# Kernel tuning notes

Measured on AMD Instinct MI355X. Metric: run time of the kernel, lower is better.

## Reference

```python
import jax, jax.numpy as jnp
import numpy as np

EMBED_DIM = 64
CODEBOOK_SIZE = 2048
COMMITMENT_COST = 1.0


def setup_inputs() -> dict:
    key = jax.random.key(0)
    k1, k2 = jax.random.split(key)
    inputs = jax.random.normal(k1, (32, 2048, EMBED_DIM), dtype=jnp.float32)
    embeddings = jax.random.normal(k2, (EMBED_DIM, CODEBOOK_SIZE), dtype=jnp.float32)
    return {"inputs": inputs, "embeddings": embeddings}


def reference(inputs, embeddings):
    # inference path (training=False): deterministic argmin quantization.
    D = embeddings.shape[0]
    K = embeddings.shape[1]
    flat = inputs.reshape(-1, D)                       # [N, D]
    similarity = flat @ embeddings                     # [N, K]
    distances = (jnp.sum(flat * flat, axis=1, keepdims=True)
                 - 2.0 * similarity
                 + jnp.sum(embeddings * embeddings, axis=0, keepdims=True))
    # gumbel layer with temperature 0 / eval mode -> argmax(-dist) == argmin(dist)
    flat_indices = jnp.argmax(-distances, axis=1)      # [N]
    encodings = jax.nn.one_hot(flat_indices, K, dtype=jnp.float32)  # [N, K]
    encoding_indices = flat_indices.reshape(inputs.shape[:-1])      # [B, T]
    quantized = jnp.take(embeddings.T, encoding_indices, axis=0)    # [B, T, D]
    e_latent_loss = jnp.mean(jnp.square(jax.lax.stop_gradient(quantized) - inputs))
    loss = e_latent_loss * COMMITMENT_COST
    return quantized, encodings, encoding_indices, loss
```

## Files before the change

kernel.cpp:

```cpp
#include <hip/hip_runtime.h>

#define N_ROWS 65536
#define DDIM   64
#define KCODES 2048
#define NB     128
#define CHUNK  256
#define NCHUNK (KCODES / CHUNK)
#define TAU    0.05f

#define Q_OFF    ((size_t)0)
#define ENC_OFF  ((size_t)N_ROWS * DDIM)
#define IDX_OFF  (ENC_OFF + (size_t)N_ROWS * KCODES)
#define LOSS_OFF (IDX_OFF + (size_t)N_ROWS)
#define INV_ND (1.0f / ((float)N_ROWS * (float)DDIM))

#define WS_ESQ_OFF   (524288)
#define WS_FLAGS_OFF (532480)

typedef __attribute__((ext_vector_type(8))) short short8;
typedef __attribute__((ext_vector_type(4))) float f32x4;

__device__ __forceinline__ unsigned short f2bf(float f) {
    unsigned u = __float_as_uint(f);
    u += 0x7FFFu + ((u >> 16) & 1u);
    return (unsigned short)(u >> 16);
}
__device__ __forceinline__ float bf2f(unsigned short h) {
    return __uint_as_float(((unsigned)h) << 16);
}

__global__ void vq_prep(const float* __restrict__ emb, char* __restrict__ ws,
                        float* __restrict__ out) {
    int t = blockIdx.x * 256 + threadIdx.x;
    int code = t & (KCODES - 1);
    int d    = t >> 11;
    float v = emb[(size_t)d * KCODES + code];
    unsigned short hi = f2bf(v);
    unsigned short lo = f2bf(v - bf2f(hi));
    int ch = code >> 8;
    int lc = code & 255;
    int kk = d ^ ((code & 7) << 3);
    short* base = (short*)ws + (size_t)ch * 32768 + lc * 64 + kk;
    base[0]     = (short)hi;
    base[16384] = (short)lo;
    if (t < KCODES) {
        float s = 0.f;
        for (int dd = 0; dd < DDIM; ++dd) {
            float e = emb[(size_t)dd * KCODES + t];
            s += e * e;
        }
        ((float*)(ws + WS_ESQ_OFF))[t] = s;
    }
    if (t == 0) out[LOSS_OFF] = 0.f;
}

__launch_bounds__(256, 2)
__global__ void vq_main(const float* __restrict__ x, const float* __restrict__ emb,
                        const char* __restrict__ ws, int* __restrict__ flags,
                        float* __restrict__ out) {
    __shared__ __align__(16) short Bs[32768];
    const int tid = threadIdx.x;
    const int l = tid & 63, w = tid >> 6;
    const int q = l >> 4, c = l & 15;
    const int r0 = blockIdx.x * NB;
    const float* esq = (const float*)(ws + WS_ESQ_OFF);

    short8 ah0[2], ah1[2], al0[2], al1[2];
    #pragma unroll
    for (int rt = 0; rt < 2; ++rt) {
        int row = r0 + w * 32 + rt * 16 + c;
        const float4* xr = (const float4*)(x + (size_t)row * DDIM);
        float4 f0 = xr[q * 2],     f1 = xr[q * 2 + 1];
        float4 f2 = xr[8 + q * 2], f3 = xr[8 + q * 2 + 1];
        float a0[8] = {f0.x,f0.y,f0.z,f0.w,f1.x,f1.y,f1.z,f1.w};
        float a1[8] = {f2.x,f2.y,f2.z,f2.w,f3.x,f3.y,f3.z,f3.w};
        #pragma unroll
        for (int j = 0; j < 8; ++j) {
            unsigned short h0 = f2bf(a0[j]);
            ah0[rt][j] = (short)h0;
            al0[rt][j] = (short)f2bf(a0[j] - bf2f(h0));
            unsigned short h1 = f2bf(a1[j]);
            ah1[rt][j] = (short)h1;
            al1[rt][j] = (short)f2bf(a1[j] - bf2f(h1));
        }
    }

    float m1[8], m2[8], m3[8]; int i1[8], i2[8];
    #pragma unroll
    for (int s = 0; s < 8; ++s) {
        m1[s] = 3.4e38f; m2[s] = 3.4e38f; m3[s] = 3.4e38f; i1[s] = 0; i2[s] = 0;
    }

    for (int ch = 0; ch < NCHUNK; ++ch) {
        const int kc = ch * CHUNK;
        __builtin_amdgcn_sched_barrier(0);
        asm volatile("s_waitcnt lgkmcnt(0)" ::: "memory");
        __builtin_amdgcn_s_barrier();
        __builtin_amdgcn_sched_barrier(0);
        {
            const int4* g4 = (const int4*)(ws + (size_t)ch * 65536);
            int4* s4 = (int4*)Bs;
            #pragma unroll
            for (int i = 0; i < 16; ++i) s4[i * 256 + tid] = g4[i * 256 + tid];
        }
        __builtin_amdgcn_sched_barrier(0);
        asm volatile("s_waitcnt lgkmcnt(0)" ::: "memory");
        __builtin_amdgcn_s_barrier();
        __builtin_amdgcn_sched_barrier(0);

        const int swz = (c & 7) << 3;
        float* ebase = out + ENC_OFF + (size_t)r0 * KCODES + kc;
        const f32x4 z = {0.f, 0.f, 0.f, 0.f};
        for (int t = 0; t < 16; ++t) {
            #pragma unroll
            for (int jj = 0; jj < 2; ++jj) {
                int s   = (t * 2 + jj) * 256 + tid;
                int row = s >> 6;
                int c4  = s & 63;
                __builtin_nontemporal_store(
                    z, (f32x4*)(ebase + (size_t)row * KCODES + (c4 << 2)));
            }
            int codeL = t * 16 + c;
            const short* ph = Bs + codeL * 64;
            const short* pl = ph + 16384;
            int k0 = (q * 8) ^ swz;
            int k1 = (32 + q * 8) ^ swz;
            short8 bh0 = *(const short8*)(ph + k0);
            short8 bh1 = *(const short8*)(ph + k1);
            short8 bl0 = *(const short8*)(pl + k0);
            short8 bl1 = *(const short8*)(pl + k1);
            int   kidx = kc + t * 16 + c;
            float eq   = esq[kidx];
            #pragma unroll
            for (int rt = 0; rt < 2; ++rt) {
                f32x4 acc = {0.f, 0.f, 0.f, 0.f};
                acc = __builtin_amdgcn_mfma_f32_16x16x32_bf16(ah0[rt], bh0, acc, 0, 0, 0);
                acc = __builtin_amdgcn_mfma_f32_16x16x32_bf16(ah1[rt], bh1, acc, 0, 0, 0);
                acc = __builtin_amdgcn_mfma_f32_16x16x32_bf16(ah0[rt], bl0, acc, 0, 0, 0);
                acc = __builtin_amdgcn_mfma_f32_16x16x32_bf16(ah1[rt], bl1, acc, 0, 0, 0);
                acc = __builtin_amdgcn_mfma_f32_16x16x32_bf16(al0[rt], bh0, acc, 0, 0, 0);
                acc = __builtin_amdgcn_mfma_f32_16x16x32_bf16(al1[rt], bh1, acc, 0, 0, 0);
                #pragma unroll
                for (int g = 0; g < 4; ++g) {
                    float dist = fmaf(-2.f, acc[g], eq);
                    int s = rt * 4 + g;
                    bool b1 = dist < m1[s];
                    bool b2 = dist < m2[s];
                    bool b3 = dist < m3[s];
                    m3[s] = b2 ? m2[s] : (b3 ? dist : m3[s]);
                    m2[s] = b1 ? m1[s] : (b2 ? dist : m2[s]);
                    i2[s] = b1 ? i1[s] : (b2 ? kidx : i2[s]);
                    m1[s] = b1 ? dist : m1[s];
                    i1[s] = b1 ? kidx : i1[s];
                }
            }
        }
    }

    __syncthreads();
    float* red  = (float*)Bs;
    int*   indS = (int*)(red + 10240);
    float* lred = red + 10240 + 128;

    #pragma unroll
    for (int rt = 0; rt < 2; ++rt)
        #pragma unroll
        for (int g = 0; g < 4; ++g) {
            int lrow = w * 32 + rt * 16 + q * 4 + g;
            float* p = red + (size_t)(lrow * 16 + c) * 5;
            int s = rt * 4 + g;
            p[0] = m1[s];
            p[1] = (float)i1[s];
            p[2] = m2[s];
            p[3] = (float)i2[s];
            p[4] = m3[s];
        }
    __syncthreads();

    if (tid < NB) {
        int row = tid;
        const float* p = red + (size_t)row * 80;
        float gm1 = 3.4e38f, gm2v = 3.4e38f, gm3 = 3.4e38f;
        int gi1 = 0x7fffffff, gi2 = 0x7fffffff;
        for (int t = 0; t < 16; ++t) {
            float v1 = p[t * 5 + 0], v2 = p[t * 5 + 2], v3 = p[t * 5 + 4];
            int   j1 = (int)p[t * 5 + 1], j2 = (int)p[t * 5 + 3];
            if (v1 < gm1 || (v1 == gm1 && j1 < gi1)) {
                gm3 = gm2v; gm2v = gm1; gi2 = gi1; gm1 = v1; gi1 = j1;
            } else if (v1 < gm2v || (v1 == gm2v && j1 < gi2)) {
                gm3 = gm2v; gm2v = v1; gi2 = j1;
            } else if (v1 < gm3) gm3 = v1;
            if (v2 < gm1 || (v2 == gm1 && j2 < gi1)) {
                gm3 = gm2v; gm2v = gm1; gi2 = gi1; gm1 = v2; gi1 = j2;
            } else if (v2 < gm2v || (v2 == gm2v && j2 < gi2)) {
                gm3 = gm2v; gm2v = v2; gi2 = j2;
            } else if (v2 < gm3) gm3 = v2;
            if (v3 < gm3) gm3 = v3;
        }
        int gr = r0 + row;
        out[IDX_OFF + gr] = (float)gi1;
        int f = 0;
        if (gm2v - gm1 < TAU) f = (gm3 - gm1 < TAU) ? 1 : ((gi2 << 2) | 2);
        flags[gr] = f;
        indS[row] = gi1;
        out[ENC_OFF + (size_t)gr * KCODES + gi1] = 1.0f;
    }
    __syncthreads();

    float lpart = 0.f;
    for (int i = tid; i < NB * (DDIM / 4); i += 256) {
        int row = i >> 4;
        int d4  = (i & 15) << 2;
        int idx = indS[row];
        int gr  = r0 + row;
        float4 qv;
        qv.x = emb[(size_t)(d4 + 0) * KCODES + idx];
        qv.y = emb[(size_t)(d4 + 1) * KCODES + idx];
        qv.z = emb[(size_t)(d4 + 2) * KCODES + idx];
        qv.w = emb[(size_t)(d4 + 3) * KCODES + idx];
        *(float4*)(out + Q_OFF + (size_t)gr * DDIM + d4) = qv;
        float4 xv = *(const float4*)(x + (size_t)gr * DDIM + d4);
        float dx = qv.x - xv.x, dy = qv.y - xv.y, dz = qv.z - xv.z, dw = qv.w - xv.w;
        lpart += dx * dx + dy * dy + dz * dz + dw * dw;
    }
    #pragma unroll
    for (int o = 32; o > 0; o >>= 1) lpart += __shfl_down(lpart, o);
    if ((tid & 63) == 0) lred[tid >> 6] = lpart;
    __syncthreads();
    if (tid == 0)
        atomicAdd(out + LOSS_OFF, (lred[0] + lred[1] + lred[2] + lred[3]) * INV_ND);
}

__global__ void vq_refine(const float* __restrict__ x, const float* __restrict__ emb,
                          const int* __restrict__ flags, float* __restrict__ out) {
    const int lane = threadIdx.x & 63;
    const int wid  = threadIdx.x >> 6;
    for (int rr = 0; rr < 8; ++rr) {
        int row = (blockIdx.x * 4 + wid) * 8 + rr;
        int f = flags[row];
        if (f == 0) continue;
        const float* xr = x + (size_t)row * DDIM;
        int oldIdx = (int)out[IDX_OFF + row];
        int bidx;
        if (f != 1) {
            int cand = f >> 2;
            double xd = (double)xr[lane];
            double ea = (double)emb[(size_t)lane * KCODES + oldIdx];
            double eb = (double)emb[(size_t)lane * KCODES + cand];
            double sa = xd * ea, sb = xd * eb;
            double qa = ea * ea, qb = eb * eb;
            #pragma unroll
            for (int o = 32; o > 0; o >>= 1) {
                sa += __shfl_down(sa, o);
                sb += __shfl_down(sb, o);
                qa += __shfl_down(qa, o);
                qb += __shfl_down(qb, o);
            }
            double dA = __shfl(qa - 2.0 * sa, 0);
            double dB = __shfl(qb - 2.0 * sb, 0);
            bidx = (dB < dA || (dB == dA && cand < oldIdx)) ? cand : oldIdx;
        } else {
            double best = 1e300; int bi = 0x7fffffff;
            for (int k = lane; k < KCODES; k += 64) {
                double s = 0.0, ee = 0.0;
                for (int d = 0; d < DDIM; ++d) {
                    double e = (double)emb[(size_t)d * KCODES + k];
                    s  = fma((double)xr[d], e, s);
                    ee = fma(e, e, ee);
                }
                double dist = ee - 2.0 * s;
                if (dist < best) { best = dist; bi = k; }
            }
            #pragma unroll
            for (int o = 32; o > 0; o >>= 1) {
                double ob = __shfl_down(best, o);
                int    oi = __shfl_down(bi, o);
                if (ob < best || (ob == best && oi < bi)) { best = ob; bi = oi; }
            }
            bidx = __shfl(bi, 0);
        }
        if (bidx == oldIdx) continue;
        if (lane == 0) {
            out[IDX_OFF + row] = (float)bidx;
            out[ENC_OFF + (size_t)row * KCODES + oldIdx] = 0.f;
            out[ENC_OFF + (size_t)row * KCODES + bidx]   = 1.f;
        }
        float eN = emb[(size_t)lane * KCODES + bidx];
        float eO = emb[(size_t)lane * KCODES + oldIdx];
        float xv = xr[lane];
        out[Q_OFF + (size_t)row * DDIM + lane] = eN;
        float dn = eN - xv, dod = eO - xv;
        float delta = dn * dn - dod * dod;
        #pragma unroll
        for (int o = 32; o > 0; o >>= 1) delta += __shfl_down(delta, o);
        if (lane == 0) atomicAdd(out + LOSS_OFF, delta * INV_ND);
    }
}

extern "C" void kernel_launch(void* const* d_in, const int* in_sizes, int n_in,
                              void* d_out, int out_size, void* d_ws, size_t ws_size,
                              hipStream_t stream) {
    const float* x   = (const float*)d_in[0];
    const float* emb = (const float*)d_in[1];
    float* out   = (float*)d_out;
    char*  ws    = (char*)d_ws;
    int*   flags = (int*)(ws + WS_FLAGS_OFF);
    hipLaunchKernelGGL(vq_prep,   dim3(512),         dim3(256), 0, stream, emb, ws, out);
    hipLaunchKernelGGL(vq_main,   dim3(N_ROWS / NB), dim3(256), 0, stream, x, emb, ws, flags, out);
    hipLaunchKernelGGL(vq_refine, dim3(N_ROWS / 32), dim3(256), 0, stream, x, emb, flags, out);
}
```

Before: 643.6 us.

## Read codebook fragments directly from global memory instead of staging through LDS

Removes the per-chunk cooperative copy of the split-bf16 codebook into a 64KB shared buffer, along with its barriers, and has each lane load its B fragments straight from the workspace via cache. Shared memory shrinks to the reduction scratch, so launch bounds are raised to allow three blocks per CU. The one-hot zero-store pattern is remapped to the full row width. The cost is global/L2 latency on every fragment load in the inner loop, with no explicit prefetching to hide it.

```diff
diff --git a/kernel.cpp b/kernel.cpp
--- a/kernel.cpp
+++ b/kernel.cpp
@@ -4,8 +4,6 @@
 #define DDIM   64
 #define KCODES 2048
 #define NB     128
-#define CHUNK  256
-#define NCHUNK (KCODES / CHUNK)
 #define TAU    0.05f
 
 #define Q_OFF    ((size_t)0)
@@ -54,16 +52,19 @@
     if (t == 0) out[LOSS_OFF] = 0.f;
 }
 
-__launch_bounds__(256, 2)
+__launch_bounds__(256, 3)
 __global__ void vq_main(const float* __restrict__ x, const float* __restrict__ emb,
                         const char* __restrict__ ws, int* __restrict__ flags,
                         float* __restrict__ out) {
-    __shared__ __align__(16) short Bs[32768];
+    __shared__ __align__(16) float red[10240];
+    __shared__ int   indS[128];
+    __shared__ float lred[4];
     const int tid = threadIdx.x;
     const int l = tid & 63, w = tid >> 6;
     const int q = l >> 4, c = l & 15;
     const int r0 = blockIdx.x * NB;
     const float* esq = (const float*)(ws + WS_ESQ_OFF);
+    const short* wsS = (const short*)ws;
 
     short8 ah0[2], ah1[2], al0[2], al1[2];
     #pragma unroll
@@ -91,76 +92,56 @@
         m1[s] = 3.4e38f; m2[s] = 3.4e38f; m3[s] = 3.4e38f; i1[s] = 0; i2[s] = 0;
     }
 
-    for (int ch = 0; ch < NCHUNK; ++ch) {
-        const int kc = ch * CHUNK;
-        __builtin_amdgcn_sched_barrier(0);
-        asm volatile("s_waitcnt lgkmcnt(0)" ::: "memory");
-        __builtin_amdgcn_s_barrier();
-        __builtin_amdgcn_sched_barrier(0);
-        {
-            const int4* g4 = (const int4*)(ws + (size_t)ch * 65536);
-            int4* s4 = (int4*)Bs;
+    const int swz = (c & 7) << 3;
+    const int k0 = (q * 8) ^ swz;
+    const int k1 = (32 + q * 8) ^ swz;
+    float* ebase = out + ENC_OFF + (size_t)r0 * KCODES;
+    const f32x4 z = {0.f, 0.f, 0.f, 0.f};
+    for (int tt = 0; tt < 128; ++tt) {
+        int code = tt * 16 + c;
+        const short* ph = wsS + (size_t)(code >> 8) * 32768 + (code & 255) * 64;
+        const short* pl = ph + 16384;
+        short8 bh0 = *(const short8*)(ph + k0);
+        short8 bh1 = *(const short8*)(ph + k1);
+        short8 bl0 = *(const short8*)(pl + k0);
+        short8 bl1 = *(const short8*)(pl + k1);
+        float eq   = esq[code];
+
+        #pragma unroll
+        for (int jj = 0; jj < 2; ++jj) {
+            int s   = (tt * 2 + jj) * 256 + tid;
+            int row = s >> 9;
+            int c4  = s & 511;
+            __builtin_nontemporal_store(
+                z, (f32x4*)(ebase + (size_t)row * KCODES + (c4 << 2)));
+        }
+
+        #pragma unroll
+        for (int rt = 0; rt < 2; ++rt) {
+            f32x4 acc = {0.f, 0.f, 0.f, 0.f};
+            acc = __builtin_amdgcn_mfma_f32_16x16x32_bf16(ah0[rt], bh0, acc, 0, 0, 0);
+            acc = __builtin_amdgcn_mfma_f32_16x16x32_bf16(ah1[rt], bh1, acc, 0, 0, 0);
+            acc = __builtin_amdgcn_mfma_f32_16x16x32_bf16(ah0[rt], bl0, acc, 0, 0, 0);
+            acc = __builtin_amdgcn_mfma_f32_16x16x32_bf16(ah1[rt], bl1, acc, 0, 0, 0);
+            acc = __builtin_amdgcn_mfma_f32_16x16x32_bf16(al0[rt], bh0, acc, 0, 0, 0);
+            acc = __builtin_amdgcn_mfma_f32_16x16x32_bf16(al1[rt], bh1, acc, 0, 0, 0);
             #pragma unroll
-            for (int i = 0; i < 16; ++i) s4[i * 256 + tid] = g4[i * 256 + tid];
-        }
-        __builtin_amdgcn_sched_barrier(0);
-        asm volatile("s_waitcnt lgkmcnt(0)" ::: "memory");
-        __builtin_amdgcn_s_barrier();
-        __builtin_amdgcn_sched_barrier(0);
-
-        const int swz = (c & 7) << 3;
-        float* ebase = out + ENC_OFF + (size_t)r0 * KCODES + kc;
-        const f32x4 z = {0.f, 0.f, 0.f, 0.f};
-        for (int t = 0; t < 16; ++t) {
-            #pragma unroll
-            for (int jj = 0; jj < 2; ++jj) {
-                int s   = (t * 2 + jj) * 256 + tid;
-                int row = s >> 6;
-                int c4  = s & 63;
-                __builtin_nontemporal_store(
-                    z, (f32x4*)(ebase + (size_t)row * KCODES + (c4 << 2)));
-            }
-            int codeL = t * 16 + c;
-            const short* ph = Bs + codeL * 64;
-            const short* pl = ph + 16384;
-            int k0 = (q * 8) ^ swz;
-            int k1 = (32 + q * 8) ^ swz;
-            short8 bh0 = *(const short8*)(ph + k0);
-            short8 bh1 = *(const short8*)(ph + k1);
-            short8 bl0 = *(const short8*)(pl + k0);
-            short8 bl1 = *(const short8*)(pl + k1);
-            int   kidx = kc + t * 16 + c;
-            float eq   = esq[kidx];
-            #pragma unroll
-            for (int rt = 0; rt < 2; ++rt) {
-                f32x4 acc = {0.f, 0.f, 0.f, 0.f};
-                acc = __builtin_amdgcn_mfma_f32_16x16x32_bf16(ah0[rt], bh0, acc, 0, 0, 0);
-                acc = __builtin_amdgcn_mfma_f32_16x16x32_bf16(ah1[rt], bh1, acc, 0, 0, 0);
-                acc = __builtin_amdgcn_mfma_f32_16x16x32_bf16(ah0[rt], bl0, acc, 0, 0, 0);
-                acc = __builtin_amdgcn_mfma_f32_16x16x32_bf16(ah1[rt], bl1, acc, 0, 0, 0);
-                acc = __builtin_amdgcn_mfma_f32_16x16x32_bf16(al0[rt], bh0, acc, 0, 0, 0);
-                acc = __builtin_amdgcn_mfma_f32_16x16x32_bf16(al1[rt], bh1, acc, 0, 0, 0);
-                #pragma unroll
-                for (int g = 0; g < 4; ++g) {
-                    float dist = fmaf(-2.f, acc[g], eq);
-                    int s = rt * 4 + g;
-                    bool b1 = dist < m1[s];
-                    bool b2 = dist < m2[s];
-                    bool b3 = dist < m3[s];
-                    m3[s] = b2 ? m2[s] : (b3 ? dist : m3[s]);
-                    m2[s] = b1 ? m1[s] : (b2 ? dist : m2[s]);
-                    i2[s] = b1 ? i1[s] : (b2 ? kidx : i2[s]);
-                    m1[s] = b1 ? dist : m1[s];
-                    i1[s] = b1 ? kidx : i1[s];
-                }
-            }
-        }
-    }
-
-    __syncthreads();
-    float* red  = (float*)Bs;
-    int*   indS = (int*)(red + 10240);
-    float* lred = red + 10240 + 128;
+            for (int g = 0; g < 4; ++g) {
+                float dist = fmaf(-2.f, acc[g], eq);
+                int s = rt * 4 + g;
+                bool b1 = dist < m1[s];
+                bool b2 = dist < m2[s];
+                bool b3 = dist < m3[s];
+                m3[s] = b2 ? m2[s] : (b3 ? dist : m3[s]);
+                m2[s] = b1 ? m1[s] : (b2 ? dist : m2[s]);
+                i2[s] = b1 ? i1[s] : (b2 ? code : i2[s]);
+                m1[s] = b1 ? dist : m1[s];
+                i1[s] = b1 ? code : i1[s];
+            }
+        }
+    }
+
+    __syncthreads();
 
     #pragma unroll
     for (int rt = 0; rt < 2; ++rt)
```

Measured after the change: 648.0 us. About the same (+0.7%).

## Halve codebook chunk and prefetch next chunk into registers during compute

Applied to the files above, without the earlier changes.

The codebook chunk size drops from 256 to 128 codes, and the next chunk is loaded from global memory into registers while the current chunk is computed, then written to LDS after a barrier. This hides global load latency that previously stalled every chunk. Code-norm values are staged in shared memory once instead of being read from global memory each step. The cost is eight extra int4 registers per thread and twice as many chunk barriers.

```diff
diff --git a/kernel.cpp b/kernel.cpp
--- a/kernel.cpp
+++ b/kernel.cpp
@@ -4,7 +4,7 @@
 #define DDIM   64
 #define KCODES 2048
 #define NB     128
-#define CHUNK  256
+#define CHUNK  128
 #define NCHUNK (KCODES / CHUNK)
 #define TAU    0.05f
 
@@ -37,12 +37,12 @@
     float v = emb[(size_t)d * KCODES + code];
     unsigned short hi = f2bf(v);
     unsigned short lo = f2bf(v - bf2f(hi));
-    int ch = code >> 8;
-    int lc = code & 255;
+    int ch = code >> 7;
+    int lc = code & 127;
     int kk = d ^ ((code & 7) << 3);
-    short* base = (short*)ws + (size_t)ch * 32768 + lc * 64 + kk;
-    base[0]     = (short)hi;
-    base[16384] = (short)lo;
+    short* base = (short*)ws + (size_t)ch * 16384 + lc * 64 + kk;
+    base[0]    = (short)hi;
+    base[8192] = (short)lo;
     if (t < KCODES) {
         float s = 0.f;
         for (int dd = 0; dd < DDIM; ++dd) {
@@ -58,12 +58,19 @@
 __global__ void vq_main(const float* __restrict__ x, const float* __restrict__ emb,
                         const char* __restrict__ ws, int* __restrict__ flags,
                         float* __restrict__ out) {
-    __shared__ __align__(16) short Bs[32768];
+    __shared__ __align__(16) char pool[41600];
+    short* Bs   = (short*)pool;
+    float* esqS = (float*)(pool + 32768);
     const int tid = threadIdx.x;
     const int l = tid & 63, w = tid >> 6;
     const int q = l >> 4, c = l & 15;
     const int r0 = blockIdx.x * NB;
-    const float* esq = (const float*)(ws + WS_ESQ_OFF);
+
+    {
+        const float4* g = (const float4*)(ws + WS_ESQ_OFF);
+        #pragma unroll
+        for (int i = 0; i < 2; ++i) ((float4*)esqS)[i * 256 + tid] = g[i * 256 + tid];
+    }
 
     short8 ah0[2], ah1[2], al0[2], al1[2];
     #pragma unroll
@@ -85,52 +92,54 @@
         }
     }
 
+    {
+        const int4* g4 = (const int4*)ws;
+        int4* s4 = (int4*)Bs;
+        #pragma unroll
+        for (int i = 0; i < 8; ++i) s4[i * 256 + tid] = g4[i * 256 + tid];
+    }
+    __syncthreads();
+
     float m1[8], m2[8], m3[8]; int i1[8], i2[8];
     #pragma unroll
     for (int s = 0; s < 8; ++s) {
         m1[s] = 3.4e38f; m2[s] = 3.4e38f; m3[s] = 3.4e38f; i1[s] = 0; i2[s] = 0;
     }
 
+    const int swz = (c & 7) << 3;
+    const int k0 = (q * 8) ^ swz;
+    const int k1 = (32 + q * 8) ^ swz;
+    int4 pf[8];
+
     for (int ch = 0; ch < NCHUNK; ++ch) {
         const int kc = ch * CHUNK;
-        __builtin_amdgcn_sched_barrier(0);
-        asm volatile("s_waitcnt lgkmcnt(0)" ::: "memory");
-        __builtin_amdgcn_s_barrier();
-        __builtin_amdgcn_sched_barrier(0);
-        {
-            const int4* g4 = (const int4*)(ws + (size_t)ch * 65536);
-            int4* s4 = (int4*)Bs;
-            #pragma unroll
-            for (int i = 0; i < 16; ++i) s4[i * 256 + tid] = g4[i * 256 + tid];
-        }
-        __builtin_amdgcn_sched_barrier(0);
-        asm volatile("s_waitcnt lgkmcnt(0)" ::: "memory");
-        __builtin_amdgcn_s_barrier();
-        __builtin_amdgcn_sched_barrier(0);
-
-        const int swz = (c & 7) << 3;
+        if (ch < NCHUNK - 1) {
+            const int4* g4 = (const int4*)(ws + (size_t)(ch + 1) * 32768);
+            #pragma unroll
+            for (int i = 0; i < 8; ++i) pf[i] = g4[i * 256 + tid];
+        }
+        __builtin_amdgcn_sched_barrier(0);
+
         float* ebase = out + ENC_OFF + (size_t)r0 * KCODES + kc;
         const f32x4 z = {0.f, 0.f, 0.f, 0.f};
-        for (int t = 0; t < 16; ++t) {
+        for (int t = 0; t < 8; ++t) {
             #pragma unroll
             for (int jj = 0; jj < 2; ++jj) {
                 int s   = (t * 2 + jj) * 256 + tid;
-                int row = s >> 6;
-                int c4  = s & 63;
+                int row = s >> 5;
+                int c4  = s & 31;
                 __builtin_nontemporal_store(
                     z, (f32x4*)(ebase + (size_t)row * KCODES + (c4 << 2)));
             }
             int codeL = t * 16 + c;
             const short* ph = Bs + codeL * 64;
-            const short* pl = ph + 16384;
-            int k0 = (q * 8) ^ swz;
-            int k1 = (32 + q * 8) ^ swz;
+            const short* pl = ph + 8192;
             short8 bh0 = *(const short8*)(ph + k0);
             short8 bh1 = *(const short8*)(ph + k1);
             short8 bl0 = *(const short8*)(pl + k0);
             short8 bl1 = *(const short8*)(pl + k1);
             int   kidx = kc + t * 16 + c;
-            float eq   = esq[kidx];
+            float eq   = esqS[kidx];
             #pragma unroll
             for (int rt = 0; rt < 2; ++rt) {
                 f32x4 acc = {0.f, 0.f, 0.f, 0.f};
@@ -155,12 +164,26 @@
                 }
             }
         }
-    }
-
-    __syncthreads();
-    float* red  = (float*)Bs;
-    int*   indS = (int*)(red + 10240);
-    float* lred = red + 10240 + 128;
+
+        __builtin_amdgcn_sched_barrier(0);
+        asm volatile("s_waitcnt lgkmcnt(0)" ::: "memory");
+        __builtin_amdgcn_s_barrier();
+        __builtin_amdgcn_sched_barrier(0);
+        if (ch < NCHUNK - 1) {
+            int4* s4 = (int4*)Bs;
+            #pragma unroll
+            for (int i = 0; i < 8; ++i) s4[i * 256 + tid] = pf[i];
+        }
+        __builtin_amdgcn_sched_barrier(0);
+        asm volatile("s_waitcnt lgkmcnt(0)" ::: "memory");
+        __builtin_amdgcn_s_barrier();
+        __builtin_amdgcn_sched_barrier(0);
+    }
+
+    __syncthreads();
+    float* red  = (float*)pool;
+    int*   indS = (int*)(pool + 40960);
+    float* lred = (float*)(pool + 41472);
 
     #pragma unroll
     for (int rt = 0; rt < 2; ++rt)
```

After: 678.7 us. +5.5%, slower.
